# Kernel optimization log

Hardware: AMD Instinct MI355X
Metric: run time of the kernel (lower is better)

## Reference

```python
import jax, jax.numpy as jnp
import numpy as np

N, E, F, DE, G, C = 50000, 800000, 64, 32, 512, 2
EPS = 1e-5


def setup_inputs() -> dict:
    key = jax.random.key(0)
    ks = jax.random.split(key, 12)
    Z = 2 * F + DE  # CGConv concat dim [x_i, x_j, edge_attr]
    inp = {
        "x": jax.random.normal(ks[0], (N, F), dtype=jnp.float32),
        "edge_index": jax.random.randint(ks[1], (2, E), 0, N, dtype=jnp.int32),
        "edge_attr": jax.random.normal(ks[2], (E, DE), dtype=jnp.float32),
        "batch": jnp.sort(jax.random.randint(ks[3], (N,), 0, G, dtype=jnp.int32)),
        # CGConv lin_f / lin_s : (2F+De) -> F, with bias
        "Wf": jax.random.normal(ks[4], (Z, F), dtype=jnp.float32) * 0.05,
        "bf": jnp.zeros((F,), dtype=jnp.float32),
        "Ws": jax.random.normal(ks[5], (Z, F), dtype=jnp.float32) * 0.05,
        "bs": jnp.zeros((F,), dtype=jnp.float32),
        # CGConv internal BatchNorm (training-mode batch stats)
        "bn_w": jnp.ones((F,), dtype=jnp.float32),
        "bn_b": jnp.zeros((F,), dtype=jnp.float32),
        # PyG LayerNorm (graph mode, batch=None -> whole-tensor stats)
        "ln_w": jnp.ones((F,), dtype=jnp.float32),
        "ln_b": jnp.zeros((F,), dtype=jnp.float32),
        # final linear (2F -> C) and output LayerNorm
        "Wl": jax.random.normal(ks[6], (2 * F, C), dtype=jnp.float32) * 0.05,
        "bl": jnp.zeros((C,), dtype=jnp.float32),
        "ln4_w": jnp.ones((C,), dtype=jnp.float32),
        "ln4_b": jnp.zeros((C,), dtype=jnp.float32),
    }
    return inp


def _pyg_layernorm(x, w, b):
    # torch_geometric.nn.LayerNorm, mode='graph', batch=None: whole-tensor stats
    xc = x - jnp.mean(x)
    out = xc / (jnp.sqrt(jnp.mean(xc * xc)) + EPS)
    return out * w + b


def reference(x, edge_index, edge_attr, batch, Wf, bf, Ws, bs, bn_w, bn_b,
              ln_w, ln_b, Wl, bl, ln4_w, ln4_b):
    src = edge_index[0]  # x_j (source)
    dst = edge_index[1]  # x_i (target / aggregation index)

    # CGConv message: sigmoid(lin_f(z)) * softplus(lin_s(z)), z=[x_i,x_j,e]
    z = jnp.concatenate([x[dst], x[src], edge_attr], axis=1)  # [E, 2F+De]
    msg = jax.nn.sigmoid(z @ Wf + bf) * jax.nn.softplus(z @ Ws + bs)  # [E,F]

    # scatter-add aggregation to target nodes
    agg = jax.ops.segment_sum(msg, dst, num_segments=N)  # [N,F]

    # CGConv batch_norm=True (training-mode batch statistics over nodes)
    mu = jnp.mean(agg, axis=0)
    var = jnp.mean((agg - mu) ** 2, axis=0)
    agg = (agg - mu) / jnp.sqrt(var + EPS) * bn_w + bn_b

    # residual
    h = agg + x

    # LayerNorm + softplus
    h = jax.nn.softplus(_pyg_layernorm(h, ln_w, ln_b))

    # global mean / add pooling over graphs
    add_pool = jax.ops.segment_sum(h, batch, num_segments=G)  # [G,F]
    counts = jax.ops.segment_sum(jnp.ones((N,), h.dtype), batch, num_segments=G)
    mean_pool = add_pool / jnp.maximum(counts, 1.0)[:, None]

    g = jnp.concatenate([mean_pool, add_pool], axis=1)  # [G, 2F]
    out = g @ Wl + bl  # [G, C]
    out = _pyg_layernorm(out, ln4_w, ln4_b)
    return out
```

## Files before the change

kernel.cpp:

```cpp
#include <hip/hip_runtime.h>
#include <math.h>

#define EPSF 1e-5f

typedef short bf16x8 __attribute__((ext_vector_type(8)));
typedef float f32x4 __attribute__((ext_vector_type(4)));

static __device__ __forceinline__ unsigned short f2bf(float x) {
  unsigned u = __float_as_uint(x);
  unsigned r = (u + 0x7FFFu + ((u >> 16) & 1u)) >> 16;
  return (unsigned short)r;
}

union BU { uint4 u; bf16x8 v; };

static __device__ __forceinline__ void gload16(const void* g, void* l) {
  __builtin_amdgcn_global_load_lds(
      (const __attribute__((address_space(1))) unsigned int*)g,
      (__attribute__((address_space(3))) unsigned int*)l, 16, 0, 0);
}

__global__ __launch_bounds__(256) void prep_kernel(
    const float* __restrict__ x, const float* __restrict__ Wf,
    const float* __restrict__ Ws, const int* __restrict__ ei,
    unsigned short* __restrict__ xbf, unsigned short* __restrict__ Bfrag,
    int* __restrict__ deg, int NCV, int total8, int E) {
  const int b = blockIdx.x, t = threadIdx.x;
  if (b < NCV) {
    int i = b * 256 + t;
    if (i < total8) {
      float4 a = ((const float4*)x)[i * 2];
      float4 c = ((const float4*)x)[i * 2 + 1];
      unsigned short o[8];
      o[0] = f2bf(a.x); o[1] = f2bf(a.y); o[2] = f2bf(a.z); o[3] = f2bf(a.w);
      o[4] = f2bf(c.x); o[5] = f2bf(c.y); o[6] = f2bf(c.z); o[7] = f2bf(c.w);
      ((uint4*)xbf)[i] = *(uint4*)o;
    }
  } else if (b < NCV + 10) {
    int g2 = (b - NCV) * 256 + t;
    if (g2 < 2560) {
      const int ks = g2 >> 9, t8 = (g2 >> 6) & 7, l = g2 & 63;
      const int q = l & 15, g = l >> 4;
      const float* W = (t8 < 4) ? Wf : Ws;
      const int col = (t8 & 3) * 16 + q;
      unsigned short out[8];
#pragma unroll
      for (int i = 0; i < 8; ++i) {
        int r = ks * 32 + g * 8 + i;
        int wr = (r < 32) ? (128 + r) : (r - 32);
        out[i] = f2bf(W[(size_t)wr * 64 + col]);
      }
      *(uint4*)&Bfrag[((size_t)(ks * 8 + t8) * 64 + l) * 8] = *(uint4*)out;
    }
  } else {
    int i = (b - NCV - 10) * 256 + t;
    if (i < E) atomicAdd(&deg[ei[E + i]], 1);
  }
}

__global__ __launch_bounds__(256) void scan_a(const int* __restrict__ deg,
                                              int* __restrict__ bsum, int N) {
  const int idx = blockIdx.x * 256 + threadIdx.x;
  int v = (idx < N) ? deg[idx] : 0;
#pragma unroll
  for (int o = 32; o > 0; o >>= 1) v += __shfl_down(v, o);
  __shared__ int ws4[4];
  if ((threadIdx.x & 63) == 0) ws4[threadIdx.x >> 6] = v;
  __syncthreads();
  if (threadIdx.x == 0) bsum[blockIdx.x] = ws4[0] + ws4[1] + ws4[2] + ws4[3];
}

__global__ __launch_bounds__(256) void scan_b(const int* __restrict__ bsum,
                                              int* __restrict__ bpre, int NB) {
  const int t = threadIdx.x;
  const int lane = t & 63, w = t >> 6;
  int v = (t < NB) ? bsum[t] : 0;
  int sc = v;
#pragma unroll
  for (int o = 1; o < 64; o <<= 1) {
    int u = __shfl_up(sc, o);
    if (lane >= o) sc += u;
  }
  __shared__ int wsum[4];
  if (lane == 63) wsum[w] = sc;
  __syncthreads();
  int add = 0;
#pragma unroll
  for (int k = 0; k < 4; ++k) add += (k < w) ? wsum[k] : 0;
  bpre[t] = (sc - v) + add;
}

__global__ __launch_bounds__(256) void scan_c(const int* __restrict__ deg,
                                              const int* __restrict__ bpre,
                                              int* __restrict__ cursor, int N) {
  const int t = threadIdx.x;
  const int lane = t & 63, w = t >> 6;
  const int idx = blockIdx.x * 256 + t;
  int d = (idx < N) ? deg[idx] : 0;
  int sc = d;
#pragma unroll
  for (int o = 1; o < 64; o <<= 1) {
    int u = __shfl_up(sc, o);
    if (lane >= o) sc += u;
  }
  __shared__ int wsum[4];
  if (lane == 63) wsum[w] = sc;
  __syncthreads();
  int add = bpre[blockIdx.x];
#pragma unroll
  for (int k = 0; k < 4; ++k) add += (k < w) ? wsum[k] : 0;
  if (idx < N) cursor[idx] = add + (sc - d);
}

__global__ __launch_bounds__(256) void scatter_pack(
    const int* __restrict__ ei, int* __restrict__ cursor,
    const float* __restrict__ eattr, int2* __restrict__ epair2,
    unsigned short* __restrict__ eabf, int E) {
  int i = blockIdx.x * 256 + threadIdx.x;
  if (i >= E) return;
  const int dst = ei[E + i];
  const int pos = atomicAdd(&cursor[dst], 1);
  epair2[pos] = make_int2(ei[i], dst);
  const float4* er = (const float4*)(eattr + (size_t)i * 32);
  unsigned short o[32];
#pragma unroll
  for (int k = 0; k < 8; ++k) {
    float4 v = er[k];
    o[k * 4] = f2bf(v.x); o[k * 4 + 1] = f2bf(v.y);
    o[k * 4 + 2] = f2bf(v.z); o[k * 4 + 3] = f2bf(v.w);
  }
  uint4* dp = (uint4*)(eabf + (size_t)pos * 32);
#pragma unroll
  for (int k = 0; k < 4; ++k) dp[k] = ((uint4*)o)[k];
}

__global__ __launch_bounds__(256, 3) void edge_fused(
    const int2* __restrict__ epair2, const unsigned short* __restrict__ eabf,
    const unsigned short* __restrict__ xbf,
    const unsigned short* __restrict__ Bfrag, const float* __restrict__ bfv_,
    const float* __restrict__ bsv_, float* __restrict__ agg, int T, int N) {
  __shared__ __align__(16) unsigned char AshB[40960];
  __shared__ __align__(16) int metaLDS[128];

  const int tt = threadIdx.x, lane = tt & 63, w = tt >> 6;
  const int q = lane & 15, g = lane >> 4;

  const int nB = gridDim.x;
  const int c = (blockIdx.x & 7) * (nB >> 3) + (blockIdx.x >> 3);
  const int q8 = T / nB, r8 = T - q8 * nB;
  const int t0 = c * q8 + min(c, r8);
  const int t1 = t0 + q8 + (c < r8 ? 1 : 0);
  if (t0 >= t1) return;

  bf16x8 Bf[5], Bs[5];
#pragma unroll
  for (int ks = 0; ks < 5; ++ks) {
    BU u1, u2;
    u1.u = ((const uint4*)Bfrag)[(ks * 8 + w) * 64 + lane];
    u2.u = ((const uint4*)Bfrag)[(ks * 8 + w + 4) * 64 + lane];
    Bf[ks] = u1.v; Bs[ks] = u2.v;
  }
  const int feat = w * 16 + q;
  const float bfv = bfv_[feat], bsv = bsv_[feat];

  int mSrc = 0, mDst = 0, nSrc = 0, nDst = 0;

  auto META = [&](int tile, int& S, int& D, int pbN) {
    int2 p = epair2[(size_t)tile * 64 + lane];
    S = p.x; D = p.y;
    int dp = __shfl_up(D, 1);
    int flag = (lane == 0 || D != dp) ? 1 : 0;
    int sc = flag;
#pragma unroll
    for (int o = 1; o < 64; o <<= 1) {
      int u = __shfl_up(sc, o);
      if (lane >= o) sc += u;
    }
    if (w == 0) metaLDS[pbN * 64 + lane] = ((sc - 1) << 20) | (D & 0xFFFFF);
  };

  auto STAGE = [&](int tile, int bufB, int S, int D) {
    const int row = (w << 4) + (lane >> 2);
    const int cx = (lane & 3) ^ ((row >> 1) & 3);
    int dR = __shfl(D, row);
    int sR = __shfl(S, row);
    unsigned du = ((unsigned)dR < (unsigned)N) ? (unsigned)dR : 0u;
    unsigned su = ((unsigned)sR < (unsigned)N) ? (unsigned)sR : 0u;
    gload16(eabf + (size_t)tile * 2048 + row * 32 + cx * 8,
            AshB + bufB + w * 1024);
    gload16(xbf + (size_t)du * 64 + cx * 8, AshB + bufB + 4096 + w * 1024);
    gload16(xbf + (size_t)du * 64 + 32 + cx * 8,
            AshB + bufB + 4096 + (w + 4) * 1024);
    gload16(xbf + (size_t)su * 64 + cx * 8, AshB + bufB + 12288 + w * 1024);
    gload16(xbf + (size_t)su * 64 + 32 + cx * 8,
            AshB + bufB + 12288 + (w + 4) * 1024);
  };

  META(t0, mSrc, mDst, 0);
  STAGE(t0, 0, mSrc, mDst);
  int pb = 0;
  for (int t = t0; t < t1; ++t) {
    const int bufC = pb * 20480;
    if (t + 1 < t1) {
      META(t + 1, nSrc, nDst, pb ^ 1);
      STAGE(t + 1, 20480 - bufC, nSrc, nDst);
    } else {
      asm volatile("s_waitcnt vmcnt(0)" ::: "memory");
    }
    asm volatile("s_waitcnt lgkmcnt(0)" ::: "memory");
    __builtin_amdgcn_sched_barrier(0);
    __builtin_amdgcn_s_barrier();
    __builtin_amdgcn_sched_barrier(0);

    f32x4 accf[4], accs[4];
#pragma unroll
    for (int mt = 0; mt < 4; ++mt) {
      accf[mt] = (f32x4){0.f, 0.f, 0.f, 0.f};
      accs[mt] = (f32x4){0.f, 0.f, 0.f, 0.f};
    }
#pragma unroll
    for (int ks = 0; ks < 5; ++ks) {
#pragma unroll
      for (int mt = 0; mt < 4; ++mt) {
        const int row = mt * 16 + q;
        const int ch = g ^ ((row >> 1) & 3);
        const bf16x8 a =
            *(const bf16x8*)(AshB + bufC + ks * 4096 + row * 64 + ch * 16);
        accf[mt] = __builtin_amdgcn_mfma_f32_16x16x32_bf16(a, Bf[ks],
                                                           accf[mt], 0, 0, 0);
        accs[mt] = __builtin_amdgcn_mfma_f32_16x16x32_bf16(a, Bs[ks],
                                                           accs[mt], 0, 0, 0);
      }
    }

#pragma unroll
    for (int mt = 0; mt < 4; ++mt) {
      const int e0 = mt * 16 + g * 4;
      const uint4 mw = *(const uint4*)&metaLDS[pb * 64 + e0];
      float mm[4];
#pragma unroll
      for (int r = 0; r < 4; ++r) {
        float F = accf[mt][r] + bfv;
        float S = accs[mt][r] + bsv;
        float sig = __builtin_amdgcn_rcpf(1.0f + __expf(-F));
        float sp = fmaxf(S, 0.f) + __logf(1.0f + __expf(-fabsf(S)));
        mm[r] = sig * sp;
      }
      const unsigned u0 = mw.x, u1 = mw.y, u2 = mw.z, u3 = mw.w;
      const unsigned d0 = u0 & 0xFFFFFu, d1 = u1 & 0xFFFFFu,
                     d2 = u2 & 0xFFFFFu, d3 = u3 & 0xFFFFFu;
      const unsigned r0 = u0 >> 20, r1 = u1 >> 20, r2 = u2 >> 20, r3 = u3 >> 20;
      float a_ = mm[0];
      unsigned cur = r0, dc = d0;
      if (r1 == cur) a_ += mm[1];
      else {
        if (dc < (unsigned)N) atomicAdd(&agg[(size_t)dc * 64 + feat], a_);
        cur = r1; dc = d1; a_ = mm[1];
      }
      if (r2 == cur) a_ += mm[2];
      else {
        if (dc < (unsigned)N) atomicAdd(&agg[(size_t)dc * 64 + feat], a_);
        cur = r2; dc = d2; a_ = mm[2];
      }
      if (r3 == cur) a_ += mm[3];
      else {
        if (dc < (unsigned)N) atomicAdd(&agg[(size_t)dc * 64 + feat], a_);
        cur = r3; dc = d3; a_ = mm[3];
      }
      if (dc < (unsigned)N) atomicAdd(&agg[(size_t)dc * 64 + feat], a_);
    }

    mSrc = nSrc; mDst = nDst;
    pb ^= 1;
    __builtin_amdgcn_s_barrier();
  }
}

__global__ __launch_bounds__(256) void stats_kernel(
    const float* __restrict__ agg, const float* __restrict__ x,
    float* __restrict__ stats, int N) {
  const int f = threadIdx.x & 63;
  const int sub = threadIdx.x >> 6;
  float sa = 0, sa2 = 0, sx = 0, sx2 = 0, sax = 0;
  for (int r = blockIdx.x * 4 + sub; r < N; r += gridDim.x * 4) {
    float a = agg[(size_t)r * 64 + f];
    float xv = x[(size_t)r * 64 + f];
    sa += a; sa2 += a * a; sx += xv; sx2 += xv * xv; sax += a * xv;
  }
  __shared__ float lds[4][5][64];
  lds[sub][0][f] = sa; lds[sub][1][f] = sa2; lds[sub][2][f] = sx;
  lds[sub][3][f] = sx2; lds[sub][4][f] = sax;
  __syncthreads();
  if (sub == 0) {
#pragma unroll
    for (int i = 0; i < 5; ++i) {
      float v = lds[0][i][f] + lds[1][i][f] + lds[2][i][f] + lds[3][i][f];
      atomicAdd(&stats[i * 64 + f], v);
    }
  }
}

__global__ __launch_bounds__(256) void node_finish(
    const float* __restrict__ stats, const float* __restrict__ bn_w,
    const float* __restrict__ bn_b, const float* __restrict__ agg,
    const float* __restrict__ x, const int* __restrict__ batch,
    const float* __restrict__ ln_w, const float* __restrict__ ln_b,
    float* __restrict__ add_pool, float* __restrict__ counts, int N,
    int chunk) {
  const int f = threadIdx.x & 63;
  const int sub = threadIdx.x >> 6;
  const float Nf = (float)N;
  const float invN = 1.0f / Nf;
  float Sa = stats[f], Sa2 = stats[64 + f], Sx = stats[128 + f],
        Sx2 = stats[192 + f], Sax = stats[256 + f];
  float mu = Sa * invN;
  float var = Sa2 * invN - mu * mu;
  const float alpha = bn_w[f] / sqrtf(var + EPSF);
  const float beta = bn_b[f] - mu * alpha;
  float Sh = alpha * Sa + Nf * beta + Sx;
  float Sh2 = alpha * alpha * Sa2 + Sx2 + Nf * beta * beta +
              2.f * alpha * Sax + 2.f * alpha * beta * Sa + 2.f * beta * Sx;
#pragma unroll
  for (int o = 32; o > 0; o >>= 1) {
    Sh += __shfl_xor(Sh, o);
    Sh2 += __shfl_xor(Sh2, o);
  }
  const float cnt = Nf * 64.0f;
  const float mean = Sh / cnt;
  const float msq = Sh2 / cnt - mean * mean;
  const float rden = 1.0f / (sqrtf(fmaxf(msq, 0.f)) + EPSF);
  const float lw = ln_w[f] * rden;
  const float lb = ln_b[f];

  const int r0 = blockIdx.x * chunk;
  const int r1 = min(N, r0 + chunk);
  float acc = 0.f, cacc = 0.f;
  int curg = -1;
  for (int r = r0 + sub; r < r1; r += 4) {
    int g = batch[r];
    if (g != curg) {
      if (curg >= 0) {
        atomicAdd(&add_pool[(size_t)curg * 64 + f], acc);
        if (f == 0) atomicAdd(&counts[curg], cacc);
      }
      curg = g; acc = 0.f; cacc = 0.f;
    }
    float h = fmaf(alpha, agg[(size_t)r * 64 + f], beta) + x[(size_t)r * 64 + f];
    float v = (h - mean) * lw + lb;
    float sp = fmaxf(v, 0.f) + __logf(1.0f + __expf(-fabsf(v)));
    acc += sp; cacc += 1.f;
  }
  if (curg >= 0) {
    atomicAdd(&add_pool[(size_t)curg * 64 + f], acc);
    if (f == 0) atomicAdd(&counts[curg], cacc);
  }
}

__global__ __launch_bounds__(1024) void graph_out(
    const float* __restrict__ add_pool, const float* __restrict__ counts,
    const float* __restrict__ Wl, const float* __restrict__ bl,
    const float* __restrict__ w4, const float* __restrict__ b4,
    float* __restrict__ out, int G) {
  const int t = threadIdx.x;
  const int g = t >> 1, c = t & 1;
  float cnt = fmaxf(counts[g], 1.0f);
  float inv = 1.0f / cnt;
  const float4* ap4 = (const float4*)(add_pool + (size_t)g * 64);
  const float4* W4 = (const float4*)Wl;
  float v = bl[c];
#pragma unroll 4
  for (int k4 = 0; k4 < 16; ++k4) {
    float4 a4 = ap4[k4];
    float4 wa = W4[k4 * 2];
    float4 wb = W4[k4 * 2 + 1];
    float4 wc = W4[32 + k4 * 2];
    float4 wd = W4[32 + k4 * 2 + 1];
    float m0 = c ? wa.y : wa.x, m1 = c ? wa.w : wa.z;
    float m2 = c ? wb.y : wb.x, m3 = c ? wb.w : wb.z;
    float a0 = c ? wc.y : wc.x, a1 = c ? wc.w : wc.z;
    float a2 = c ? wd.y : wd.x, a3 = c ? wd.w : wd.z;
    v = fmaf(a4.x, fmaf(m0, inv, a0), v);
    v = fmaf(a4.y, fmaf(m1, inv, a1), v);
    v = fmaf(a4.z, fmaf(m2, inv, a2), v);
    v = fmaf(a4.w, fmaf(m3, inv, a3), v);
  }

  __shared__ float red[16];
  __shared__ float bc[2];
  float sum = v;
#pragma unroll
  for (int o = 32; o > 0; o >>= 1) sum += __shfl_down(sum, o);
  if ((t & 63) == 0) red[t >> 6] = sum;
  __syncthreads();
  if (t == 0) {
    float tot = 0;
#pragma unroll
    for (int i = 0; i < 16; ++i) tot += red[i];
    bc[0] = tot * (1.0f / 1024.0f);
  }
  __syncthreads();
  const float mean = bc[0];
  const float xc = v - mean;
  float sq = xc * xc;
  __syncthreads();
#pragma unroll
  for (int o = 32; o > 0; o >>= 1) sq += __shfl_down(sq, o);
  if ((t & 63) == 0) red[t >> 6] = sq;
  __syncthreads();
  if (t == 0) {
    float tot = 0;
#pragma unroll
    for (int i = 0; i < 16; ++i) tot += red[i];
    bc[1] = 1.0f / (sqrtf(tot * (1.0f / 1024.0f)) + EPSF);
  }
  __syncthreads();
  out[t] = xc * bc[1] * w4[c] + b4[c];
}

extern "C" void kernel_launch(void* const* d_in, const int* in_sizes, int n_in,
                              void* d_out, int out_size, void* d_ws,
                              size_t ws_size, hipStream_t stream) {
  const float* x = (const float*)d_in[0];
  const int* ei = (const int*)d_in[1];
  const float* eattr = (const float*)d_in[2];
  const int* batch = (const int*)d_in[3];
  const float* Wf = (const float*)d_in[4];
  const float* bf = (const float*)d_in[5];
  const float* Ws = (const float*)d_in[6];
  const float* bs = (const float*)d_in[7];
  const float* bn_w = (const float*)d_in[8];
  const float* bn_b = (const float*)d_in[9];
  const float* ln_w = (const float*)d_in[10];
  const float* ln_b = (const float*)d_in[11];
  const float* Wl = (const float*)d_in[12];
  const float* bl = (const float*)d_in[13];
  const float* w4 = (const float*)d_in[14];
  const float* b4 = (const float*)d_in[15];

  const int N = in_sizes[0] / 64;
  const int E = in_sizes[2] / 32;
  const int G = 512;
  const int NB = (N + 255) / 256;
  const int T = (E + 63) / 64;
  const int NCV = (N * 8 + 255) / 256;
  const int NH = (E + 255) / 256;

  float* ws = (float*)d_ws;
  float* agg = ws;
  float* stats = agg + (size_t)N * 64;
  float* add_pool = stats + 320;
  float* counts = add_pool + (size_t)G * 64;
  int* deg = (int*)(counts + G);
  int* cursor = deg + N;
  int* bsum = cursor + N;
  int* bpre = bsum + 256;
  unsigned short* Bfrag = (unsigned short*)(bpre + 256);
  unsigned short* xbf = Bfrag + 20480;
  unsigned short* eabf = xbf + (size_t)N * 64;
  int2* epair2 = (int2*)(eabf + (size_t)T * 2048);

  size_t zeroFloats = (size_t)N * 64 + 320 + (size_t)G * 64 + G + N;
  hipMemsetAsync(agg, 0, zeroFloats * sizeof(float), stream);
  const int padE = T * 64 - E;
  if (padE > 0) hipMemsetAsync(epair2 + E, 0xFF, (size_t)padE * 8, stream);

  prep_kernel<<<NCV + 10 + NH, 256, 0, stream>>>(x, Wf, Ws, ei, xbf, Bfrag,
                                                 deg, NCV, N * 8, E);
  scan_a<<<NB, 256, 0, stream>>>(deg, bsum, N);
  scan_b<<<1, 256, 0, stream>>>(bsum, bpre, NB);
  scan_c<<<NB, 256, 0, stream>>>(deg, bpre, cursor, N);
  scatter_pack<<<NH, 256, 0, stream>>>(ei, cursor, eattr, epair2, eabf, E);
  edge_fused<<<768, 256, 0, stream>>>(epair2, eabf, xbf, Bfrag, bf, bs, agg, T,
                                      N);
  stats_kernel<<<512, 256, 0, stream>>>(agg, x, stats, N);
  const int chunk = (N + 511) / 512;
  node_finish<<<512, 256, 0, stream>>>(stats, bn_w, bn_b, agg, x, batch, ln_w,
                                       ln_b, add_pool, counts, N, chunk);
  graph_out<<<1, 1024, 0, stream>>>(add_pool, counts, Wl, bl, w4, b4,
                                    (float*)d_out, G);
}
```

Baseline: 329.2 us.

## Precompute per-node destination projection and drop x_i from per-edge GEMM

Splits the linear layer algebraically so the x_dst contribution (plus bias) is computed once per node in a new fp32 node_gemm kernel. The edge kernel then adds it during the epilogue, which shrinks the edge GEMM K from 160 to 96 and cuts gathered bytes and LDS per tile. The smaller LDS footprint allows occupancy 4 and a 1280-block grid, and the prefetch/barrier schedule is restructured. In exchange it adds an extra kernel, an N×128 fp32 buffer, and per-segment gathers of Pdst in the epilogue. The x_dst term is now kept in fp32 rather than bf16.

```diff
diff --git a/kernel.cpp b/kernel.cpp
--- a/kernel.cpp
+++ b/kernel.cpp
@@ -18,6 +18,33 @@
   __builtin_amdgcn_global_load_lds(
       (const __attribute__((address_space(1))) unsigned int*)g,
       (__attribute__((address_space(3))) unsigned int*)l, 16, 0, 0);
+}
+
+__global__ __launch_bounds__(256) void node_gemm(
+    const float* __restrict__ x, const float* __restrict__ Wf,
+    const float* __restrict__ bf, const float* __restrict__ Ws,
+    const float* __restrict__ bs, float* __restrict__ Pdst, int N) {
+  const int lane = threadIdx.x & 63;
+  const int w = threadIdx.x >> 6;
+  const int part = w & 1, half = w >> 1;
+  const float* W = part ? Ws : Wf;
+  float wreg[64];
+#pragma unroll
+  for (int k = 0; k < 64; ++k) wreg[k] = W[k * 64 + lane];
+  const float bias = part ? bs[lane] : bf[lane];
+  for (int n = blockIdx.x * 2 + half; n < N; n += gridDim.x * 2) {
+    const float* xr = x + (size_t)n * 64;
+    float acc = bias;
+#pragma unroll
+    for (int k = 0; k < 64; k += 4) {
+      float4 xv = *(const float4*)(xr + k);
+      acc = fmaf(xv.x, wreg[k], acc);
+      acc = fmaf(xv.y, wreg[k + 1], acc);
+      acc = fmaf(xv.z, wreg[k + 2], acc);
+      acc = fmaf(xv.w, wreg[k + 3], acc);
+    }
+    Pdst[(size_t)n * 128 + part * 64 + lane] = acc;
+  }
 }
 
 __global__ __launch_bounds__(256) void prep_kernel(
@@ -36,9 +63,9 @@
       o[4] = f2bf(c.x); o[5] = f2bf(c.y); o[6] = f2bf(c.z); o[7] = f2bf(c.w);
       ((uint4*)xbf)[i] = *(uint4*)o;
     }
-  } else if (b < NCV + 10) {
+  } else if (b < NCV + 6) {
     int g2 = (b - NCV) * 256 + t;
-    if (g2 < 2560) {
+    if (g2 < 1536) {
       const int ks = g2 >> 9, t8 = (g2 >> 6) & 7, l = g2 & 63;
       const int q = l & 15, g = l >> 4;
       const float* W = (t8 < 4) ? Wf : Ws;
@@ -46,14 +73,14 @@
       unsigned short out[8];
 #pragma unroll
       for (int i = 0; i < 8; ++i) {
-        int r = ks * 32 + g * 8 + i;
-        int wr = (r < 32) ? (128 + r) : (r - 32);
+        int kk = ks * 32 + g * 8 + i;
+        int wr = (kk < 32) ? (128 + kk) : (32 + kk);
         out[i] = f2bf(W[(size_t)wr * 64 + col]);
       }
       *(uint4*)&Bfrag[((size_t)(ks * 8 + t8) * 64 + l) * 8] = *(uint4*)out;
     }
   } else {
-    int i = (b - NCV - 10) * 256 + t;
+    int i = (b - NCV - 6) * 256 + t;
     if (i < E) atomicAdd(&deg[ei[E + i]], 1);
   }
 }
@@ -134,13 +161,13 @@
   for (int k = 0; k < 4; ++k) dp[k] = ((uint4*)o)[k];
 }
 
-__global__ __launch_bounds__(256, 3) void edge_fused(
+__global__ __launch_bounds__(256, 4) void edge_fused(
     const int2* __restrict__ epair2, const unsigned short* __restrict__ eabf,
     const unsigned short* __restrict__ xbf,
-    const unsigned short* __restrict__ Bfrag, const float* __restrict__ bfv_,
-    const float* __restrict__ bsv_, float* __restrict__ agg, int T, int N) {
-  __shared__ __align__(16) unsigned char AshB[40960];
-  __shared__ __align__(16) int metaLDS[128];
+    const unsigned short* __restrict__ Bfrag, const float* __restrict__ Pdst,
+    float* __restrict__ agg, int T, int N) {
+  __shared__ __align__(16) unsigned char AshB[2][12288];
+  __shared__ __align__(16) int metaLDS[2][64];
 
   const int tt = threadIdx.x, lane = tt & 63, w = tt >> 6;
   const int q = lane & 15, g = lane >> 4;
@@ -152,66 +179,57 @@
   const int t1 = t0 + q8 + (c < r8 ? 1 : 0);
   if (t0 >= t1) return;
 
-  bf16x8 Bf[5], Bs[5];
-#pragma unroll
-  for (int ks = 0; ks < 5; ++ks) {
+  bf16x8 Bf[3], Bs[3];
+#pragma unroll
+  for (int ks = 0; ks < 3; ++ks) {
     BU u1, u2;
     u1.u = ((const uint4*)Bfrag)[(ks * 8 + w) * 64 + lane];
     u2.u = ((const uint4*)Bfrag)[(ks * 8 + w + 4) * 64 + lane];
     Bf[ks] = u1.v; Bs[ks] = u2.v;
   }
   const int feat = w * 16 + q;
-  const float bfv = bfv_[feat], bsv = bsv_[feat];
-
-  int mSrc = 0, mDst = 0, nSrc = 0, nDst = 0;
-
-  auto META = [&](int tile, int& S, int& D, int pbN) {
-    int2 p = epair2[(size_t)tile * 64 + lane];
-    S = p.x; D = p.y;
-    int dp = __shfl_up(D, 1);
-    int flag = (lane == 0 || D != dp) ? 1 : 0;
-    int sc = flag;
-#pragma unroll
-    for (int o = 1; o < 64; o <<= 1) {
-      int u = __shfl_up(sc, o);
-      if (lane >= o) sc += u;
-    }
-    if (w == 0) metaLDS[pbN * 64 + lane] = ((sc - 1) << 20) | (D & 0xFFFFF);
+
+  auto SCAN = [&](int D, int slot) {
+    if (w == 0) {
+      int dp = __shfl_up(D, 1);
+      int flag = (lane == 0 || D != dp) ? 1 : 0;
+      int sc = flag;
+#pragma unroll
+      for (int o = 1; o < 64; o <<= 1) {
+        int u = __shfl_up(sc, o);
+        if (lane >= o) sc += u;
+      }
+      metaLDS[slot][lane] = ((sc - 1) << 20) | (D & 0xFFFFF);
+    }
   };
 
-  auto STAGE = [&](int tile, int bufB, int S, int D) {
+  auto STAGE = [&](int tile, int bufSel, int Sreg) {
     const int row = (w << 4) + (lane >> 2);
-    const int cx = (lane & 3) ^ ((row >> 1) & 3);
-    int dR = __shfl(D, row);
-    int sR = __shfl(S, row);
-    unsigned du = ((unsigned)dR < (unsigned)N) ? (unsigned)dR : 0u;
-    unsigned su = ((unsigned)sR < (unsigned)N) ? (unsigned)sR : 0u;
-    gload16(eabf + (size_t)tile * 2048 + row * 32 + cx * 8,
-            AshB + bufB + w * 1024);
-    gload16(xbf + (size_t)du * 64 + cx * 8, AshB + bufB + 4096 + w * 1024);
-    gload16(xbf + (size_t)du * 64 + 32 + cx * 8,
-            AshB + bufB + 4096 + (w + 4) * 1024);
-    gload16(xbf + (size_t)su * 64 + cx * 8, AshB + bufB + 12288 + w * 1024);
-    gload16(xbf + (size_t)su * 64 + 32 + cx * 8,
-            AshB + bufB + 12288 + (w + 4) * 1024);
+    const int sw = (row ^ (row >> 2)) & 3;
+    const int cc = (lane & 3) ^ sw;
+    int sR = __shfl(Sreg, row);
+    unsigned su = min((unsigned)sR, (unsigned)(N - 1));
+    char* buf = (char*)&AshB[bufSel][0] + w * 1024;
+    gload16(eabf + (size_t)tile * 2048 + row * 32 + cc * 8, buf);
+    gload16(xbf + (size_t)su * 64 + cc * 8, buf + 4096);
+    gload16(xbf + (size_t)su * 64 + 32 + cc * 8, buf + 8192);
   };
 
-  META(t0, mSrc, mDst, 0);
-  STAGE(t0, 0, mSrc, mDst);
+  {
+    int2 p0 = epair2[(size_t)t0 * 64 + lane];
+    SCAN(p0.y, 0);
+    STAGE(t0, 0, p0.x);
+  }
+  int2 pn = make_int2(0, -1);
+  if (t0 + 1 < t1) pn = epair2[(size_t)(t0 + 1) * 64 + lane];
+  asm volatile("s_waitcnt vmcnt(0)" ::: "memory");
+  __builtin_amdgcn_sched_barrier(0);
+  __builtin_amdgcn_s_barrier();
+  __builtin_amdgcn_sched_barrier(0);
+
   int pb = 0;
   for (int t = t0; t < t1; ++t) {
-    const int bufC = pb * 20480;
-    if (t + 1 < t1) {
-      META(t + 1, nSrc, nDst, pb ^ 1);
-      STAGE(t + 1, 20480 - bufC, nSrc, nDst);
-    } else {
-      asm volatile("s_waitcnt vmcnt(0)" ::: "memory");
-    }
-    asm volatile("s_waitcnt lgkmcnt(0)" ::: "memory");
-    __builtin_amdgcn_sched_barrier(0);
-    __builtin_amdgcn_s_barrier();
-    __builtin_amdgcn_sched_barrier(0);
-
+    const char* bufc = (const char*)&AshB[0][0] + pb * 12288;
     f32x4 accf[4], accs[4];
 #pragma unroll
     for (int mt = 0; mt < 4; ++mt) {
@@ -219,13 +237,13 @@
       accs[mt] = (f32x4){0.f, 0.f, 0.f, 0.f};
     }
 #pragma unroll
-    for (int ks = 0; ks < 5; ++ks) {
+    for (int ks = 0; ks < 3; ++ks) {
 #pragma unroll
       for (int mt = 0; mt < 4; ++mt) {
         const int row = mt * 16 + q;
-        const int ch = g ^ ((row >> 1) & 3);
+        const int sw = (row ^ (row >> 2)) & 3;
         const bf16x8 a =
-            *(const bf16x8*)(AshB + bufC + ks * 4096 + row * 64 + ch * 16);
+            *(const bf16x8*)(bufc + ks * 4096 + row * 64 + ((g ^ sw) << 4));
         accf[mt] = __builtin_amdgcn_mfma_f32_16x16x32_bf16(a, Bf[ks],
                                                            accf[mt], 0, 0, 0);
         accs[mt] = __builtin_amdgcn_mfma_f32_16x16x32_bf16(a, Bs[ks],
@@ -233,46 +251,52 @@
       }
     }
 
+    if (t + 1 < t1) {
+      SCAN(pn.y, pb ^ 1);
+      STAGE(t + 1, pb ^ 1, pn.x);
+      if (t + 2 < t1) pn = epair2[(size_t)(t + 2) * 64 + lane];
+    }
+
 #pragma unroll
     for (int mt = 0; mt < 4; ++mt) {
       const int e0 = mt * 16 + g * 4;
-      const uint4 mw = *(const uint4*)&metaLDS[pb * 64 + e0];
-      float mm[4];
-#pragma unroll
-      for (int r = 0; r < 4; ++r) {
-        float F = accf[mt][r] + bfv;
-        float S = accs[mt][r] + bsv;
-        float sig = __builtin_amdgcn_rcpf(1.0f + __expf(-F));
-        float sp = fmaxf(S, 0.f) + __logf(1.0f + __expf(-fabsf(S)));
-        mm[r] = sig * sp;
-      }
-      const unsigned u0 = mw.x, u1 = mw.y, u2 = mw.z, u3 = mw.w;
-      const unsigned d0 = u0 & 0xFFFFFu, d1 = u1 & 0xFFFFFu,
-                     d2 = u2 & 0xFFFFFu, d3 = u3 & 0xFFFFFu;
-      const unsigned r0 = u0 >> 20, r1 = u1 >> 20, r2 = u2 >> 20, r3 = u3 >> 20;
-      float a_ = mm[0];
-      unsigned cur = r0, dc = d0;
-      if (r1 == cur) a_ += mm[1];
-      else {
-        if (dc < (unsigned)N) atomicAdd(&agg[(size_t)dc * 64 + feat], a_);
-        cur = r1; dc = d1; a_ = mm[1];
-      }
-      if (r2 == cur) a_ += mm[2];
-      else {
-        if (dc < (unsigned)N) atomicAdd(&agg[(size_t)dc * 64 + feat], a_);
-        cur = r2; dc = d2; a_ = mm[2];
-      }
-      if (r3 == cur) a_ += mm[3];
-      else {
-        if (dc < (unsigned)N) atomicAdd(&agg[(size_t)dc * 64 + feat], a_);
-        cur = r3; dc = d3; a_ = mm[3];
-      }
-      if (dc < (unsigned)N) atomicAdd(&agg[(size_t)dc * 64 + feat], a_);
-    }
-
-    mSrc = nSrc; mDst = nDst;
+      const uint4 mw = *(const uint4*)&metaLDS[pb][e0];
+      unsigned cur = mw.x >> 20;
+      unsigned d = mw.x & 0xFFFFFu;
+      unsigned dl = min(d, (unsigned)(N - 1));
+      float pf = Pdst[(size_t)dl * 128 + feat];
+      float ps = Pdst[(size_t)dl * 128 + 64 + feat];
+      float F = accf[mt][0] + pf;
+      float Sv = accs[mt][0] + ps;
+      float a_ = __builtin_amdgcn_rcpf(1.0f + __expf(-F)) *
+                 (fmaxf(Sv, 0.f) + __logf(1.0f + __expf(-fabsf(Sv))));
+#define STEP(UU, RIDX)                                                        \
+  {                                                                           \
+    unsigned rr = (UU) >> 20;                                                 \
+    if (rr != cur) {                                                          \
+      if (d < (unsigned)N) atomicAdd(&agg[(size_t)d * 64 + feat], a_);        \
+      cur = rr; d = (UU) & 0xFFFFFu; dl = min(d, (unsigned)(N - 1));          \
+      pf = Pdst[(size_t)dl * 128 + feat];                                     \
+      ps = Pdst[(size_t)dl * 128 + 64 + feat];                                \
+      a_ = 0.f;                                                               \
+    }                                                                         \
+    float F2 = accf[mt][RIDX] + pf;                                           \
+    float S2 = accs[mt][RIDX] + ps;                                           \
+    a_ += __builtin_amdgcn_rcpf(1.0f + __expf(-F2)) *                         \
+          (fmaxf(S2, 0.f) + __logf(1.0f + __expf(-fabsf(S2))));               \
+  }
+      STEP(mw.y, 1)
+      STEP(mw.z, 2)
+      STEP(mw.w, 3)
+#undef STEP
+      if (d < (unsigned)N) atomicAdd(&agg[(size_t)d * 64 + feat], a_);
+    }
+
+    asm volatile("s_waitcnt vmcnt(0)" ::: "memory");
+    __builtin_amdgcn_sched_barrier(0);
+    __builtin_amdgcn_s_barrier();
+    __builtin_amdgcn_sched_barrier(0);
     pb ^= 1;
-    __builtin_amdgcn_s_barrier();
   }
 }
 
@@ -455,8 +479,9 @@
   int* bsum = cursor + N;
   int* bpre = bsum + 256;
   unsigned short* Bfrag = (unsigned short*)(bpre + 256);
-  unsigned short* xbf = Bfrag + 20480;
-  unsigned short* eabf = xbf + (size_t)N * 64;
+  unsigned short* xbf = Bfrag + 12288;
+  float* Pdst = (float*)(xbf + (size_t)N * 64);
+  unsigned short* eabf = (unsigned short*)(Pdst + (size_t)N * 128);
   int2* epair2 = (int2*)(eabf + (size_t)T * 2048);
 
   size_t zeroFloats = (size_t)N * 64 + 320 + (size_t)G * 64 + G + N;
@@ -464,14 +489,15 @@
   const int padE = T * 64 - E;
   if (padE > 0) hipMemsetAsync(epair2 + E, 0xFF, (size_t)padE * 8, stream);
 
-  prep_kernel<<<NCV + 10 + NH, 256, 0, stream>>>(x, Wf, Ws, ei, xbf, Bfrag,
-                                                 deg, NCV, N * 8, E);
+  prep_kernel<<<NCV + 6 + NH, 256, 0, stream>>>(x, Wf, Ws, ei, xbf, Bfrag, deg,
+                                                NCV, N * 8, E);
+  node_gemm<<<2048, 256, 0, stream>>>(x, Wf, bf, Ws, bs, Pdst, N);
   scan_a<<<NB, 256, 0, stream>>>(deg, bsum, N);
   scan_b<<<1, 256, 0, stream>>>(bsum, bpre, NB);
   scan_c<<<NB, 256, 0, stream>>>(deg, bpre, cursor, N);
   scatter_pack<<<NH, 256, 0, stream>>>(ei, cursor, eattr, epair2, eabf, E);
-  edge_fused<<<768, 256, 0, stream>>>(epair2, eabf, xbf, Bfrag, bf, bs, agg, T,
-                                      N);
+  edge_fused<<<1280, 256, 0, stream>>>(epair2, eabf, xbf, Bfrag, Pdst, agg, T,
+                                       N);
   stats_kernel<<<512, 256, 0, stream>>>(agg, x, stats, N);
   const int chunk = (N + 511) / 512;
   node_finish<<<512, 256, 0, stream>>>(stats, bn_w, bn_b, agg, x, batch, ln_w,
```

Result: slower. 393.1 us (+19.4%).

## Precompute destination-node projection per node and shrink edge GEMM to edge+source

Applied to the files above, without the earlier changes.

The x_i (destination) part of the linear layers is split out. A new node_mfma kernel computes x@W_dst plus the biases once per node into a fp32 Pdst buffer. The edge kernel then only multiplies the edge attributes and source features (K=96 instead of 160), and adds the gathered Pdst values per destination row before the activation. The edge kernel is also restructured to per-wave 16-edge tiles, with B fragments held in LDS and register double-buffered direct global loads instead of LDS staging through global_load_lds. This removes redundant per-edge work for destination features at the cost of an extra node pass, an fp32 gather of Pdst per destination run, and a different occupancy/grid configuration.

```diff
diff --git a/kernel.cpp b/kernel.cpp
--- a/kernel.cpp
+++ b/kernel.cpp
@@ -12,19 +12,18 @@
   return (unsigned short)r;
 }
 
-union BU { uint4 u; bf16x8 v; };
-
-static __device__ __forceinline__ void gload16(const void* g, void* l) {
-  __builtin_amdgcn_global_load_lds(
-      (const __attribute__((address_space(1))) unsigned int*)g,
-      (__attribute__((address_space(3))) unsigned int*)l, 16, 0, 0);
+static __device__ __forceinline__ float msgv(float F, float S) {
+  float sig = __builtin_amdgcn_rcpf(1.0f + __expf(-F));
+  float sp = fmaxf(S, 0.f) + __logf(1.0f + __expf(-fabsf(S)));
+  return sig * sp;
 }
 
 __global__ __launch_bounds__(256) void prep_kernel(
     const float* __restrict__ x, const float* __restrict__ Wf,
     const float* __restrict__ Ws, const int* __restrict__ ei,
     unsigned short* __restrict__ xbf, unsigned short* __restrict__ Bfrag,
-    int* __restrict__ deg, int NCV, int total8, int E) {
+    unsigned short* __restrict__ Bfrag2, int* __restrict__ deg, int NCV,
+    int total8, int E) {
   const int b = blockIdx.x, t = threadIdx.x;
   if (b < NCV) {
     int i = b * 256 + t;
@@ -36,9 +35,9 @@
       o[4] = f2bf(c.x); o[5] = f2bf(c.y); o[6] = f2bf(c.z); o[7] = f2bf(c.w);
       ((uint4*)xbf)[i] = *(uint4*)o;
     }
-  } else if (b < NCV + 10) {
+  } else if (b < NCV + 6) {
     int g2 = (b - NCV) * 256 + t;
-    if (g2 < 2560) {
+    if (g2 < 1536) {
       const int ks = g2 >> 9, t8 = (g2 >> 6) & 7, l = g2 & 63;
       const int q = l & 15, g = l >> 4;
       const float* W = (t8 < 4) ? Wf : Ws;
@@ -46,15 +45,73 @@
       unsigned short out[8];
 #pragma unroll
       for (int i = 0; i < 8; ++i) {
-        int r = ks * 32 + g * 8 + i;
-        int wr = (r < 32) ? (128 + r) : (r - 32);
+        int kk = ks * 32 + g * 8 + i;
+        int wr = (kk < 32) ? (128 + kk) : (32 + kk);
         out[i] = f2bf(W[(size_t)wr * 64 + col]);
       }
       *(uint4*)&Bfrag[((size_t)(ks * 8 + t8) * 64 + l) * 8] = *(uint4*)out;
     }
+  } else if (b < NCV + 10) {
+    int g2 = (b - NCV - 6) * 256 + t;
+    if (g2 < 1024) {
+      const int ks = g2 >> 9, t8 = (g2 >> 6) & 7, l = g2 & 63;
+      const int q = l & 15, g = l >> 4;
+      const float* W = (t8 < 4) ? Wf : Ws;
+      const int col = (t8 & 3) * 16 + q;
+      unsigned short out[8];
+#pragma unroll
+      for (int i = 0; i < 8; ++i) {
+        int kk = ks * 32 + g * 8 + i;
+        out[i] = f2bf(W[(size_t)kk * 64 + col]);
+      }
+      *(uint4*)&Bfrag2[((size_t)(ks * 8 + t8) * 64 + l) * 8] = *(uint4*)out;
+    }
   } else {
     int i = (b - NCV - 10) * 256 + t;
     if (i < E) atomicAdd(&deg[ei[E + i]], 1);
+  }
+}
+
+__global__ __launch_bounds__(256, 4) void node_mfma(
+    const unsigned short* __restrict__ xbf,
+    const unsigned short* __restrict__ Bfrag2, const float* __restrict__ bf_,
+    const float* __restrict__ bs_, float* __restrict__ Pdst, int N) {
+  __shared__ __align__(16) short Bsh[16][64][8];
+  for (int i = threadIdx.x; i < 1024; i += 256)
+    ((uint4*)Bsh)[i] = ((const uint4*)Bfrag2)[i];
+  __syncthreads();
+  const int lane = threadIdx.x & 63, w = threadIdx.x >> 6;
+  const int q = lane & 15, g = lane >> 4;
+  const int row0 = blockIdx.x * 64;
+  const float bfv = bf_[w * 16 + q], bsv = bs_[w * 16 + q];
+  f32x4 accf[4], accs[4];
+#pragma unroll
+  for (int mt = 0; mt < 4; ++mt) {
+    accf[mt] = (f32x4){0.f, 0.f, 0.f, 0.f};
+    accs[mt] = (f32x4){0.f, 0.f, 0.f, 0.f};
+  }
+#pragma unroll
+  for (int ks = 0; ks < 2; ++ks) {
+    const bf16x8 Bfr = *(const bf16x8*)&Bsh[ks * 8 + w][lane][0];
+    const bf16x8 Bsr = *(const bf16x8*)&Bsh[ks * 8 + 4 + w][lane][0];
+#pragma unroll
+    for (int mt = 0; mt < 4; ++mt) {
+      int row = min(row0 + mt * 16 + q, N - 1);
+      const bf16x8 a = *(const bf16x8*)(xbf + (size_t)row * 64 + ks * 32 + g * 8);
+      accf[mt] = __builtin_amdgcn_mfma_f32_16x16x32_bf16(a, Bfr, accf[mt], 0, 0, 0);
+      accs[mt] = __builtin_amdgcn_mfma_f32_16x16x32_bf16(a, Bsr, accs[mt], 0, 0, 0);
+    }
+  }
+#pragma unroll
+  for (int mt = 0; mt < 4; ++mt) {
+#pragma unroll
+    for (int r = 0; r < 4; ++r) {
+      int row = row0 + mt * 16 + g * 4 + r;
+      if (row < N) {
+        Pdst[(size_t)row * 128 + w * 16 + q] = accf[mt][r] + bfv;
+        Pdst[(size_t)row * 128 + 64 + w * 16 + q] = accs[mt][r] + bsv;
+      }
+    }
   }
 }
 
@@ -134,145 +191,100 @@
   for (int k = 0; k < 4; ++k) dp[k] = ((uint4*)o)[k];
 }
 
-__global__ __launch_bounds__(256, 3) void edge_fused(
+__global__ __launch_bounds__(256, 4) void edge_fused(
     const int2* __restrict__ epair2, const unsigned short* __restrict__ eabf,
     const unsigned short* __restrict__ xbf,
-    const unsigned short* __restrict__ Bfrag, const float* __restrict__ bfv_,
-    const float* __restrict__ bsv_, float* __restrict__ agg, int T, int N) {
-  __shared__ __align__(16) unsigned char AshB[40960];
-  __shared__ __align__(16) int metaLDS[128];
-
-  const int tt = threadIdx.x, lane = tt & 63, w = tt >> 6;
+    const unsigned short* __restrict__ Bfrag, const float* __restrict__ Pdst,
+    float* __restrict__ agg, int T16, int N) {
+  __shared__ __align__(16) short Bsh[24][64][8];
+  for (int i = threadIdx.x; i < 1536; i += 256)
+    ((uint4*)Bsh)[i] = ((const uint4*)Bfrag)[i];
+  __syncthreads();
+
+  const int lane = threadIdx.x & 63, w = threadIdx.x >> 6;
   const int q = lane & 15, g = lane >> 4;
 
   const int nB = gridDim.x;
-  const int c = (blockIdx.x & 7) * (nB >> 3) + (blockIdx.x >> 3);
-  const int q8 = T / nB, r8 = T - q8 * nB;
-  const int t0 = c * q8 + min(c, r8);
-  const int t1 = t0 + q8 + (c < r8 ? 1 : 0);
-  if (t0 >= t1) return;
-
-  bf16x8 Bf[5], Bs[5];
-#pragma unroll
-  for (int ks = 0; ks < 5; ++ks) {
-    BU u1, u2;
-    u1.u = ((const uint4*)Bfrag)[(ks * 8 + w) * 64 + lane];
-    u2.u = ((const uint4*)Bfrag)[(ks * 8 + w + 4) * 64 + lane];
-    Bf[ks] = u1.v; Bs[ks] = u2.v;
-  }
-  const int feat = w * 16 + q;
-  const float bfv = bfv_[feat], bsv = bsv_[feat];
-
-  int mSrc = 0, mDst = 0, nSrc = 0, nDst = 0;
-
-  auto META = [&](int tile, int& S, int& D, int pbN) {
-    int2 p = epair2[(size_t)tile * 64 + lane];
-    S = p.x; D = p.y;
-    int dp = __shfl_up(D, 1);
-    int flag = (lane == 0 || D != dp) ? 1 : 0;
-    int sc = flag;
-#pragma unroll
-    for (int o = 1; o < 64; o <<= 1) {
-      int u = __shfl_up(sc, o);
-      if (lane >= o) sc += u;
-    }
-    if (w == 0) metaLDS[pbN * 64 + lane] = ((sc - 1) << 20) | (D & 0xFFFFF);
-  };
-
-  auto STAGE = [&](int tile, int bufB, int S, int D) {
-    const int row = (w << 4) + (lane >> 2);
-    const int cx = (lane & 3) ^ ((row >> 1) & 3);
-    int dR = __shfl(D, row);
-    int sR = __shfl(S, row);
-    unsigned du = ((unsigned)dR < (unsigned)N) ? (unsigned)dR : 0u;
-    unsigned su = ((unsigned)sR < (unsigned)N) ? (unsigned)sR : 0u;
-    gload16(eabf + (size_t)tile * 2048 + row * 32 + cx * 8,
-            AshB + bufB + w * 1024);
-    gload16(xbf + (size_t)du * 64 + cx * 8, AshB + bufB + 4096 + w * 1024);
-    gload16(xbf + (size_t)du * 64 + 32 + cx * 8,
-            AshB + bufB + 4096 + (w + 4) * 1024);
-    gload16(xbf + (size_t)su * 64 + cx * 8, AshB + bufB + 12288 + w * 1024);
-    gload16(xbf + (size_t)su * 64 + 32 + cx * 8,
-            AshB + bufB + 12288 + (w + 4) * 1024);
-  };
-
-  META(t0, mSrc, mDst, 0);
-  STAGE(t0, 0, mSrc, mDst);
-  int pb = 0;
-  for (int t = t0; t < t1; ++t) {
-    const int bufC = pb * 20480;
-    if (t + 1 < t1) {
-      META(t + 1, nSrc, nDst, pb ^ 1);
-      STAGE(t + 1, 20480 - bufC, nSrc, nDst);
-    } else {
-      asm volatile("s_waitcnt vmcnt(0)" ::: "memory");
-    }
-    asm volatile("s_waitcnt lgkmcnt(0)" ::: "memory");
-    __builtin_amdgcn_sched_barrier(0);
-    __builtin_amdgcn_s_barrier();
-    __builtin_amdgcn_sched_barrier(0);
+  const int cb = (blockIdx.x & 7) * (nB >> 3) + (blockIdx.x >> 3);
+  const int q8 = T16 / nB, r8 = T16 - q8 * nB;
+  const int t0 = cb * q8 + min(cb, r8);
+  const int t1 = t0 + q8 + (cb < r8 ? 1 : 0);
+
+  int t = t0 + w;
+  if (t >= t1) return;
+
+  int2 p = epair2[(size_t)t * 16 + q];
+  bf16x8 aE = *(const bf16x8*)(eabf + (size_t)t * 512 + q * 32 + g * 8);
+  unsigned su = min((unsigned)p.x, (unsigned)(N - 1));
+  bf16x8 aX0 = *(const bf16x8*)(xbf + (size_t)su * 64 + g * 8);
+  bf16x8 aX1 = *(const bf16x8*)(xbf + (size_t)su * 64 + 32 + g * 8);
+
+  while (true) {
+    const int tn = t + 4;
+    const bool more = (tn < t1);
+    int2 pn = p;
+    bf16x8 aEn = aE, aX0n = aX0, aX1n = aX1;
+    if (more) {
+      pn = epair2[(size_t)tn * 16 + q];
+      aEn = *(const bf16x8*)(eabf + (size_t)tn * 512 + q * 32 + g * 8);
+      unsigned sn = min((unsigned)pn.x, (unsigned)(N - 1));
+      aX0n = *(const bf16x8*)(xbf + (size_t)sn * 64 + g * 8);
+      aX1n = *(const bf16x8*)(xbf + (size_t)sn * 64 + 32 + g * 8);
+    }
 
     f32x4 accf[4], accs[4];
 #pragma unroll
-    for (int mt = 0; mt < 4; ++mt) {
-      accf[mt] = (f32x4){0.f, 0.f, 0.f, 0.f};
-      accs[mt] = (f32x4){0.f, 0.f, 0.f, 0.f};
-    }
-#pragma unroll
-    for (int ks = 0; ks < 5; ++ks) {
-#pragma unroll
-      for (int mt = 0; mt < 4; ++mt) {
-        const int row = mt * 16 + q;
-        const int ch = g ^ ((row >> 1) & 3);
-        const bf16x8 a =
-            *(const bf16x8*)(AshB + bufC + ks * 4096 + row * 64 + ch * 16);
-        accf[mt] = __builtin_amdgcn_mfma_f32_16x16x32_bf16(a, Bf[ks],
-                                                           accf[mt], 0, 0, 0);
-        accs[mt] = __builtin_amdgcn_mfma_f32_16x16x32_bf16(a, Bs[ks],
-                                                           accs[mt], 0, 0, 0);
-      }
-    }
-
-#pragma unroll
-    for (int mt = 0; mt < 4; ++mt) {
-      const int e0 = mt * 16 + g * 4;
-      const uint4 mw = *(const uint4*)&metaLDS[pb * 64 + e0];
-      float mm[4];
-#pragma unroll
-      for (int r = 0; r < 4; ++r) {
-        float F = accf[mt][r] + bfv;
-        float S = accs[mt][r] + bsv;
-        float sig = __builtin_amdgcn_rcpf(1.0f + __expf(-F));
-        float sp = fmaxf(S, 0.f) + __logf(1.0f + __expf(-fabsf(S)));
-        mm[r] = sig * sp;
-      }
-      const unsigned u0 = mw.x, u1 = mw.y, u2 = mw.z, u3 = mw.w;
-      const unsigned d0 = u0 & 0xFFFFFu, d1 = u1 & 0xFFFFFu,
-                     d2 = u2 & 0xFFFFFu, d3 = u3 & 0xFFFFFu;
-      const unsigned r0 = u0 >> 20, r1 = u1 >> 20, r2 = u2 >> 20, r3 = u3 >> 20;
-      float a_ = mm[0];
-      unsigned cur = r0, dc = d0;
-      if (r1 == cur) a_ += mm[1];
-      else {
-        if (dc < (unsigned)N) atomicAdd(&agg[(size_t)dc * 64 + feat], a_);
-        cur = r1; dc = d1; a_ = mm[1];
-      }
-      if (r2 == cur) a_ += mm[2];
-      else {
-        if (dc < (unsigned)N) atomicAdd(&agg[(size_t)dc * 64 + feat], a_);
-        cur = r2; dc = d2; a_ = mm[2];
-      }
-      if (r3 == cur) a_ += mm[3];
-      else {
-        if (dc < (unsigned)N) atomicAdd(&agg[(size_t)dc * 64 + feat], a_);
-        cur = r3; dc = d3; a_ = mm[3];
-      }
+    for (int nt = 0; nt < 4; ++nt) {
+      f32x4 z = {0.f, 0.f, 0.f, 0.f};
+      accf[nt] = __builtin_amdgcn_mfma_f32_16x16x32_bf16(
+          aE, *(const bf16x8*)&Bsh[nt][lane][0], z, 0, 0, 0);
+      accf[nt] = __builtin_amdgcn_mfma_f32_16x16x32_bf16(
+          aX0, *(const bf16x8*)&Bsh[8 + nt][lane][0], accf[nt], 0, 0, 0);
+      accf[nt] = __builtin_amdgcn_mfma_f32_16x16x32_bf16(
+          aX1, *(const bf16x8*)&Bsh[16 + nt][lane][0], accf[nt], 0, 0, 0);
+      f32x4 z2 = {0.f, 0.f, 0.f, 0.f};
+      accs[nt] = __builtin_amdgcn_mfma_f32_16x16x32_bf16(
+          aE, *(const bf16x8*)&Bsh[4 + nt][lane][0], z2, 0, 0, 0);
+      accs[nt] = __builtin_amdgcn_mfma_f32_16x16x32_bf16(
+          aX0, *(const bf16x8*)&Bsh[12 + nt][lane][0], accs[nt], 0, 0, 0);
+      accs[nt] = __builtin_amdgcn_mfma_f32_16x16x32_bf16(
+          aX1, *(const bf16x8*)&Bsh[20 + nt][lane][0], accs[nt], 0, 0, 0);
+    }
+
+    int d0 = __shfl(p.y, g * 4);
+    int d1 = __shfl(p.y, g * 4 + 1);
+    int d2 = __shfl(p.y, g * 4 + 2);
+    int d3 = __shfl(p.y, g * 4 + 3);
+#pragma unroll
+    for (int cg = 0; cg < 4; ++cg) {
+      const int feat = cg * 16 + q;
+      const float* Pf = Pdst + feat;
+      unsigned dc = (unsigned)d0;
+      unsigned dl = min(dc, (unsigned)(N - 1));
+      float pf = Pf[(size_t)dl * 128];
+      float ps = Pf[(size_t)dl * 128 + 64];
+      float a_ = msgv(accf[cg][0] + pf, accs[cg][0] + ps);
+#define STEP(DR, RIDX)                                                        \
+  {                                                                           \
+    unsigned dr = (unsigned)(DR);                                             \
+    if (dr != dc) {                                                           \
+      if (dc < (unsigned)N) atomicAdd(&agg[(size_t)dc * 64 + feat], a_);      \
+      dc = dr; dl = min(dc, (unsigned)(N - 1));                               \
+      pf = Pf[(size_t)dl * 128];                                              \
+      ps = Pf[(size_t)dl * 128 + 64];                                         \
+      a_ = 0.f;                                                               \
+    }                                                                         \
+    a_ += msgv(accf[cg][RIDX] + pf, accs[cg][RIDX] + ps);                     \
+  }
+      STEP(d1, 1)
+      STEP(d2, 2)
+      STEP(d3, 3)
+#undef STEP
       if (dc < (unsigned)N) atomicAdd(&agg[(size_t)dc * 64 + feat], a_);
     }
 
-    mSrc = nSrc; mDst = nDst;
-    pb ^= 1;
-    __builtin_amdgcn_s_barrier();
+    if (!more) break;
+    p = pn; aE = aEn; aX0 = aX0n; aX1 = aX1n; t = tn;
   }
 }
 
@@ -441,7 +453,7 @@
   const int E = in_sizes[2] / 32;
   const int G = 512;
   const int NB = (N + 255) / 256;
-  const int T = (E + 63) / 64;
+  const int T16 = (E + 15) / 16;
   const int NCV = (N * 8 + 255) / 256;
   const int NH = (E + 255) / 256;
 
@@ -455,23 +467,26 @@
   int* bsum = cursor + N;
   int* bpre = bsum + 256;
   unsigned short* Bfrag = (unsigned short*)(bpre + 256);
-  unsigned short* xbf = Bfrag + 20480;
-  unsigned short* eabf = xbf + (size_t)N * 64;
-  int2* epair2 = (int2*)(eabf + (size_t)T * 2048);
+  unsigned short* Bfrag2 = Bfrag + 12288;
+  unsigned short* xbf = Bfrag2 + 8192;
+  float* Pdst = (float*)(xbf + (size_t)N * 64);
+  unsigned short* eabf = (unsigned short*)(Pdst + (size_t)N * 128);
+  int2* epair2 = (int2*)(eabf + (size_t)T16 * 512);
 
   size_t zeroFloats = (size_t)N * 64 + 320 + (size_t)G * 64 + G + N;
   hipMemsetAsync(agg, 0, zeroFloats * sizeof(float), stream);
-  const int padE = T * 64 - E;
+  const int padE = T16 * 16 - E;
   if (padE > 0) hipMemsetAsync(epair2 + E, 0xFF, (size_t)padE * 8, stream);
 
   prep_kernel<<<NCV + 10 + NH, 256, 0, stream>>>(x, Wf, Ws, ei, xbf, Bfrag,
-                                                 deg, NCV, N * 8, E);
+                                                 Bfrag2, deg, NCV, N * 8, E);
+  node_mfma<<<(N + 63) / 64, 256, 0, stream>>>(xbf, Bfrag2, bf, bs, Pdst, N);
   scan_a<<<NB, 256, 0, stream>>>(deg, bsum, N);
   scan_b<<<1, 256, 0, stream>>>(bsum, bpre, NB);
   scan_c<<<NB, 256, 0, stream>>>(deg, bpre, cursor, N);
   scatter_pack<<<NH, 256, 0, stream>>>(ei, cursor, eattr, epair2, eabf, E);
-  edge_fused<<<768, 256, 0, stream>>>(epair2, eabf, xbf, Bfrag, bf, bs, agg, T,
-                                      N);
+  edge_fused<<<1024, 256, 0, stream>>>(epair2, eabf, xbf, Bfrag, Pdst, agg,
+                                       T16, N);
   stats_kernel<<<512, 256, 0, stream>>>(agg, x, stats, N);
   const int chunk = (N + 511) / 512;
   node_finish<<<512, 256, 0, stream>>>(stats, bn_w, bn_b, agg, x, batch, ln_w,
```

Result: slower. 380.8 us (+15.7%).
